# Performance work log

Measured on AMD Instinct MI355X. Metric: run time of the kernel, lower is better.

The kernel has to match this reference:

```python
import jax, jax.numpy as jnp
import numpy as np

D_MODEL = 1024
HIDDEN = 1024
N_EXPERTS = 8
TOP_K = 2
BATCH, SEQ = 2, 2048
N_TOKENS = BATCH * SEQ


def setup_inputs() -> dict:
    key = jax.random.key(0)
    ks = jax.random.split(key, 6)
    x = jax.random.normal(ks[0], (BATCH, SEQ, D_MODEL), dtype=jnp.float32)
    expert_weights = jax.random.uniform(ks[1], (N_TOKENS, TOP_K), dtype=jnp.float32)
    expert_indices = jax.random.randint(ks[2], (N_TOKENS, TOP_K), 0, N_EXPERTS, dtype=jnp.int32)
    s_in = 1.0 / np.sqrt(D_MODEL)
    s_hid = 1.0 / np.sqrt(HIDDEN)
    w1 = jax.random.normal(ks[3], (N_EXPERTS, D_MODEL, HIDDEN), dtype=jnp.float32) * s_in
    w3 = jax.random.normal(ks[4], (N_EXPERTS, D_MODEL, HIDDEN), dtype=jnp.float32) * s_in
    w2 = jax.random.normal(ks[5], (N_EXPERTS, HIDDEN, D_MODEL), dtype=jnp.float32) * s_hid
    return {"x": x, "expert_weights": expert_weights, "expert_indices": expert_indices,
            "w1": w1, "w3": w3, "w2": w2}


def reference(x, expert_weights, expert_indices, w1, w3, w2):
    """Dropless MoE MLP (forward_once path): for each token t,
    out[t] = sum_k expert_weights[t,k] * SwiGLU_{expert_indices[t,k]}(x[t]).
    Also returns batch_size_per_expert (histogram of routed assignments).
    """
    d = x.shape[-1]
    xf = x.reshape(-1, d)                                  # [N, d]
    E = w1.shape[0]
    # combine[t, e] = sum over top-k slots routed to expert e of their weight
    onehot = jax.nn.one_hot(expert_indices, E, dtype=xf.dtype)       # [N, K, E]
    combine = jnp.einsum("nk,nke->ne", expert_weights, onehot)      # [N, E]
    out = jnp.zeros_like(xf)
    for e in range(E):  # fixed small loop over experts
        h = jax.nn.silu(xf @ w1[e]) * (xf @ w3[e])          # [N, H]
        out = out + combine[:, e:e + 1] * (h @ w2[e])       # [N, d]
    batch_size_per_expert = jnp.zeros((E,), dtype=jnp.int32).at[
        expert_indices.reshape(-1)].add(1)
    return out.reshape(x.shape), batch_size_per_expert
```

## Files before the change

kernel.cpp:

```cpp
#include <hip/hip_runtime.h>
#include <cstdint>

#define D 1024
#define N_TOKENS 4096
#define N_SLOTS 8192
#define NEXP 8
#define NKT 16
#define MAXT 80
#define NTRF 8

typedef float f32x4 __attribute__((ext_vector_type(4)));
typedef __bf16 bf16x8 __attribute__((ext_vector_type(8)));
typedef __attribute__((address_space(3))) uint32_t lds_u32;
typedef __attribute__((address_space(1))) const uint32_t glb_u32;

__device__ __forceinline__ void gload_lds16(const void* g, void* l) {
  __builtin_amdgcn_global_load_lds((glb_u32*)g, (lds_u32*)l, 16, 0, 0);
}

__device__ __forceinline__ ushort f2bf(float f) {
  union { float f; uint32_t u; } c; c.f = f;
  uint32_t u = c.u;
  return (ushort)((u + 0x7FFFu + ((u >> 16) & 1u)) >> 16);
}

__device__ __forceinline__ float bf2f(ushort u) {
  union { uint32_t u; float f; } c; c.u = (uint32_t)u << 16;
  return c.f;
}

__device__ __forceinline__ bf16x8 lds_frag(const ushort* base, int row, int s) {
  return *(const bf16x8*)((const char*)base + row * 128 + ((s ^ (row & 7)) * 16));
}

#define TPAD 66

__global__ void prep_k(const float* __restrict__ x, const int* __restrict__ ei,
                       const float* __restrict__ ew,
                       const float* __restrict__ w1, const float* __restrict__ w3,
                       float* __restrict__ hist_out, int* __restrict__ meta,
                       int* __restrict__ tok, int* __restrict__ smap,
                       ushort* __restrict__ Xbf, ushort* __restrict__ w13t) {
  int bid = blockIdx.x, t = threadIdx.x;
  if (bid == 0) {
    __shared__ int cmat[256][8];
    __shared__ int off[NEXP + 1];
#pragma unroll
    for (int e = 0; e < NEXP; e++) cmat[t][e] = 0;
    int base = t * 32;
#pragma unroll 4
    for (int j = 0; j < 32; j++) cmat[t][ei[base + j]]++;
    __syncthreads();
    if (t < NEXP) {
      int run = 0;
      for (int i = 0; i < 256; i++) { int v = cmat[i][t]; cmat[i][t] = run; run += v; }
      meta[8 + t] = run;
    }
    __syncthreads();
    if (t == 0) {
      int s = 0;
      for (int e = 0; e < NEXP; e++) { off[e] = s; s += meta[8 + e]; }
      off[NEXP] = s;
      int nt = 0;
      for (int e = 0; e < NEXP; e++)
        for (int r = off[e]; r < off[e + 1]; r += 128)
          if (nt < MAXT) {
            meta[16 + nt] = e;
            meta[96 + nt] = r;
            int re = off[e + 1]; if (r + 128 < re) re = r + 128;
            meta[176 + nt] = re;
            nt++;
          }
      meta[0] = nt;
      for (int e = 0; e < NEXP; e++) hist_out[e] = (float)meta[8 + e];
    }
    __syncthreads();
#pragma unroll 4
    for (int j = 0; j < 32; j++) {
      int slot = base + j;
      int e = ei[slot];
      int p = off[e] + cmat[t][e]++;
      tok[p] = slot >> 1;
      smap[slot] = p;
    }
  } else if (bid <= 256) {
    int cb = bid - 1;
    const float4* xs = (const float4*)x + (size_t)cb * 4096;
    ushort4* xd = (ushort4*)Xbf + (size_t)cb * 4096;
#pragma unroll
    for (int i = 0; i < 16; i++) {
      float4 v = xs[i * 256 + t];
      ushort4 o;
      o.x = f2bf(v.x); o.y = f2bf(v.y); o.z = f2bf(v.z); o.w = f2bf(v.w);
      xd[i * 256 + t] = o;
    }
  } else {
    int wb = bid - 257;
    int z = wb >> 8, rem = wb & 255;
    int kb = rem >> 4, nb = rem & 15;
    int which = z >> 3, e = z & 7;
    const float* src = (which == 0 ? w1 : w3) + (size_t)e * D * D;
    ushort* dst = w13t + (size_t)e * 2048 * D;
    __shared__ ushort tile[64][TPAD];
    int k0 = kb * 64, n0 = nb * 64;
    int r = t >> 4, c = t & 15;
#pragma unroll
    for (int rep = 0; rep < 4; rep++) {
      int krow = rep * 16 + r;
      float4 v = *(const float4*)(src + (size_t)(k0 + krow) * D + n0 + c * 4);
      tile[krow][c * 4 + 0] = f2bf(v.x);
      tile[krow][c * 4 + 1] = f2bf(v.y);
      tile[krow][c * 4 + 2] = f2bf(v.z);
      tile[krow][c * 4 + 3] = f2bf(v.w);
    }
    __syncthreads();
#pragma unroll
    for (int rep = 0; rep < 4; rep++) {
      int lr = rep * 16 + r;
      int nrow = n0 + lr;
      ushort4 o;
      o.x = tile[c * 4 + 0][lr];
      o.y = tile[c * 4 + 1][lr];
      o.z = tile[c * 4 + 2][lr];
      o.w = tile[c * 4 + 3][lr];
      int crow = ((nrow >> 4) << 5) + ((which == 1) ? 16 : 0) + (nrow & 15);
      *(ushort4*)(dst + (size_t)crow * D + k0 + c * 4) = o;
    }
  }
}

__global__ __launch_bounds__(256, 4) void gemm1_k(
    const ushort* __restrict__ Xbf, const ushort* __restrict__ W13t,
    ushort* __restrict__ H, const int* __restrict__ tok,
    const int* __restrict__ meta,
    const float* __restrict__ w2, ushort* __restrict__ W2t) {
  __shared__ ushort sA[128 * 64];
  __shared__ ushort sB[128 * 64];
  int tm = blockIdx.y;
  int tid = threadIdx.x;

  if (tm < NTRF) {
    int gid = tm * 16 + blockIdx.x;
    int e = gid >> 4, kb = gid & 15;
    const float* src = w2 + (size_t)e * D * D;
    ushort* dst = W2t + (size_t)e * D * D;
    ushort (*tile)[TPAD] = (ushort(*)[TPAD])&sA[0];
    int r = tid >> 4, c = tid & 15;
    int k0 = kb * 64;
    const float* sp = src + (size_t)k0 * D + c * 4;
    float4 va[4], vb[4];
#pragma unroll
    for (int rep = 0; rep < 4; rep++)
      va[rep] = *(const float4*)(sp + (size_t)(rep * 16 + r) * D);
    for (int i = 0; i < 16; i += 2) {
      __syncthreads();
#pragma unroll
      for (int rep = 0; rep < 4; rep++) {
        int krow = rep * 16 + r;
        tile[krow][c * 4 + 0] = f2bf(va[rep].x);
        tile[krow][c * 4 + 1] = f2bf(va[rep].y);
        tile[krow][c * 4 + 2] = f2bf(va[rep].z);
        tile[krow][c * 4 + 3] = f2bf(va[rep].w);
      }
      if (i + 1 < 16)
#pragma unroll
        for (int rep = 0; rep < 4; rep++)
          vb[rep] = *(const float4*)(sp + (size_t)(rep * 16 + r) * D + (i + 1) * 64);
      __syncthreads();
      {
        int n0 = i * 64;
#pragma unroll
        for (int rep = 0; rep < 4; rep++) {
          int lr = rep * 16 + r;
          ushort4 o;
          o.x = tile[c * 4 + 0][lr];
          o.y = tile[c * 4 + 1][lr];
          o.z = tile[c * 4 + 2][lr];
          o.w = tile[c * 4 + 3][lr];
          *(ushort4*)(dst + (size_t)(n0 + lr) * D + k0 + c * 4) = o;
        }
      }
      __syncthreads();
#pragma unroll
      for (int rep = 0; rep < 4; rep++) {
        int krow = rep * 16 + r;
        tile[krow][c * 4 + 0] = f2bf(vb[rep].x);
        tile[krow][c * 4 + 1] = f2bf(vb[rep].y);
        tile[krow][c * 4 + 2] = f2bf(vb[rep].z);
        tile[krow][c * 4 + 3] = f2bf(vb[rep].w);
      }
      if (i + 2 < 16)
#pragma unroll
        for (int rep = 0; rep < 4; rep++)
          va[rep] = *(const float4*)(sp + (size_t)(rep * 16 + r) * D + (i + 2) * 64);
      __syncthreads();
      {
        int n0 = (i + 1) * 64;
#pragma unroll
        for (int rep = 0; rep < 4; rep++) {
          int lr = rep * 16 + r;
          ushort4 o;
          o.x = tile[c * 4 + 0][lr];
          o.y = tile[c * 4 + 1][lr];
          o.z = tile[c * 4 + 2][lr];
          o.w = tile[c * 4 + 3][lr];
          *(ushort4*)(dst + (size_t)(n0 + lr) * D + k0 + c * 4) = o;
        }
      }
    }
    return;
  }
  tm -= NTRF;
  if (tm >= meta[0]) return;

  int e = meta[16 + tm], r0 = meta[96 + tm], rend = meta[176 + tm];
  int n0i = blockIdx.x * 128;
  int lane = tid & 63, wid = tid >> 6;
  int wm = wid >> 1, wn = wid & 1;

  const char* gX = (const char*)Xbf;
  const char* gB = (const char*)(W13t + (size_t)e * 2048 * D);

  int prow = tid >> 3, pslot = tid & 7;
  size_t arow[4];
  int brow[4], phys[4];
#pragma unroll
  for (int i = 0; i < 4; i++) {
    int row = i * 32 + prow;
    int gr = r0 + row; if (gr > N_SLOTS - 1) gr = N_SLOTS - 1;
    arow[i] = (size_t)tok[gr] * 2048;
    brow[i] = n0i + row;
    phys[i] = (pslot ^ (row & 7)) * 16;
  }

  f32x4 acc[4][4] = {};

  for (int kt = 0; kt < NKT; kt++) {
    int kb = kt * 128;
#pragma unroll
    for (int i = 0; i < 4; i++) {
      gload_lds16(gX + arow[i] + kb + phys[i], (char*)sA + (i * 256 + tid) * 16);
      gload_lds16(gB + (size_t)brow[i] * 2048 + kb + phys[i],
                  (char*)sB + (i * 256 + tid) * 16);
    }
    __syncthreads();
#pragma unroll
    for (int kk = 0; kk < 2; kk++) {
      int s = kk * 4 + (lane >> 4);
      bf16x8 a[4], b[4];
#pragma unroll
      for (int mf = 0; mf < 4; mf++)
        a[mf] = lds_frag(sA, wm * 64 + mf * 16 + (lane & 15), s);
#pragma unroll
      for (int nf = 0; nf < 4; nf++)
        b[nf] = lds_frag(sB, wn * 64 + nf * 16 + (lane & 15), s);
#pragma unroll
      for (int mf = 0; mf < 4; mf++)
#pragma unroll
        for (int nf = 0; nf < 4; nf++)
          acc[mf][nf] = __builtin_amdgcn_mfma_f32_16x16x32_bf16(a[mf], b[nf], acc[mf][nf], 0, 0, 0);
    }
    __syncthreads();
  }

  int cb = (n0i >> 1) + wn * 32 + (lane & 15);
#pragma unroll
  for (int mf = 0; mf < 4; mf++)
#pragma unroll
    for (int v = 0; v < 4; v++) {
      int r = r0 + wm * 64 + mf * 16 + (lane >> 4) * 4 + v;
      if (r >= rend) continue;
#pragma unroll
      for (int p = 0; p < 2; p++) {
        float g = acc[mf][2 * p][v], u = acc[mf][2 * p + 1][v];
        float hv = g / (1.f + __expf(-g)) * u;
        H[(size_t)r * D + cb + p * 16] = f2bf(hv);
      }
    }
}

__global__ __launch_bounds__(256, 4) void gemm2_k(
    const ushort* __restrict__ Hm, const ushort* __restrict__ W2t,
    ushort* __restrict__ Y, const int* __restrict__ meta) {
  __shared__ ushort sA[128 * 64];
  __shared__ ushort sB[128 * 64];
  int tm = blockIdx.y;
  if (tm >= meta[0]) return;
  int e = meta[16 + tm], r0 = meta[96 + tm], rend = meta[176 + tm];
  int n0 = blockIdx.x * 128;
  int tid = threadIdx.x, lane = tid & 63, wid = tid >> 6;
  int wm = wid >> 1, wn = wid & 1;

  const char* gH = (const char*)Hm;
  const char* gB = (const char*)(W2t + (size_t)e * D * D);

  int prow = tid >> 3, pslot = tid & 7;
  size_t arow[4];
  int brow[4], phys[4];
#pragma unroll
  for (int i = 0; i < 4; i++) {
    int row = i * 32 + prow;
    int gr = r0 + row; if (gr > N_SLOTS - 1) gr = N_SLOTS - 1;
    arow[i] = (size_t)gr * 2048;
    brow[i] = n0 + row;
    phys[i] = (pslot ^ (row & 7)) * 16;
  }

  f32x4 acc[4][4] = {};

  for (int kt = 0; kt < NKT; kt++) {
    int kb = kt * 128;
#pragma unroll
    for (int i = 0; i < 4; i++) {
      gload_lds16(gH + arow[i] + kb + phys[i], (char*)sA + (i * 256 + tid) * 16);
      gload_lds16(gB + (size_t)brow[i] * 2048 + kb + phys[i],
                  (char*)sB + (i * 256 + tid) * 16);
    }
    __syncthreads();
#pragma unroll
    for (int kk = 0; kk < 2; kk++) {
      int s = kk * 4 + (lane >> 4);
      bf16x8 a[4], b[4];
#pragma unroll
      for (int mf = 0; mf < 4; mf++)
        a[mf] = lds_frag(sA, wm * 64 + mf * 16 + (lane & 15), s);
#pragma unroll
      for (int nf = 0; nf < 4; nf++)
        b[nf] = lds_frag(sB, wn * 64 + nf * 16 + (lane & 15), s);
#pragma unroll
      for (int mf = 0; mf < 4; mf++)
#pragma unroll
        for (int nf = 0; nf < 4; nf++)
          acc[mf][nf] = __builtin_amdgcn_mfma_f32_16x16x32_bf16(a[mf], b[nf], acc[mf][nf], 0, 0, 0);
    }
    __syncthreads();
  }

#pragma unroll
  for (int mf = 0; mf < 4; mf++)
#pragma unroll
    for (int v = 0; v < 4; v++) {
      int r = r0 + wm * 64 + mf * 16 + (lane >> 4) * 4 + v;
      if (r >= rend) continue;
#pragma unroll
      for (int nf = 0; nf < 4; nf++)
        Y[(size_t)r * D + n0 + wn * 64 + nf * 16 + (lane & 15)] = f2bf(acc[mf][nf][v]);
    }
}

__global__ void combine_k(const ushort* __restrict__ Y, const int* __restrict__ smap,
                          const float* __restrict__ ew, float* __restrict__ out) {
  int tkn = blockIdx.x * 4 + (threadIdx.x >> 6);
  int lane = threadIdx.x & 63;
  int p0 = smap[2 * tkn], p1 = smap[2 * tkn + 1];
  float w0 = ew[2 * tkn], w1 = ew[2 * tkn + 1];
  const ushort4* y0 = (const ushort4*)(Y + (size_t)p0 * D);
  const ushort4* y1 = (const ushort4*)(Y + (size_t)p1 * D);
  float4* o = (float4*)(out + (size_t)tkn * D);
#pragma unroll
  for (int j = 0; j < 4; j++) {
    int c = j * 64 + lane;
    ushort4 a = y0[c], b = y1[c];
    float4 v;
    v.x = w0 * bf2f(a.x) + w1 * bf2f(b.x);
    v.y = w0 * bf2f(a.y) + w1 * bf2f(b.y);
    v.z = w0 * bf2f(a.z) + w1 * bf2f(b.z);
    v.w = w0 * bf2f(a.w) + w1 * bf2f(b.w);
    o[c] = v;
  }
}

extern "C" void kernel_launch(void* const* d_in, const int* in_sizes, int n_in,
                              void* d_out, int out_size, void* d_ws, size_t ws_size,
                              hipStream_t stream) {
  const float* x  = (const float*)d_in[0];
  const float* ew = (const float*)d_in[1];
  const int*   ei = (const int*)d_in[2];
  const float* w1 = (const float*)d_in[3];
  const float* w3 = (const float*)d_in[4];
  const float* w2 = (const float*)d_in[5];
  float* out = (float*)d_out;

  char* ws = (char*)d_ws;
  int*    meta = (int*)ws;
  int*    tok  = (int*)(ws + 4096);
  int*    smap = (int*)(ws + 4096 + 32768);
  ushort* Xbf  = (ushort*)(ws + (1ull << 20));
  ushort* W13t = (ushort*)(ws + (9ull << 20));
  ushort* W2t  = (ushort*)(ws + (41ull << 20));
  ushort* Hm   = (ushort*)(ws + (57ull << 20));
  ushort* Ym   = (ushort*)(ws + (1ull << 20));

  prep_k<<<4353, 256, 0, stream>>>(x, ei, ew, w1, w3,
                                   out + (size_t)N_TOKENS * D, meta, tok, smap,
                                   Xbf, W13t);
  gemm1_k<<<dim3(16, NTRF + MAXT), 256, 0, stream>>>(Xbf, W13t, Hm, tok, meta, w2, W2t);
  gemm2_k<<<dim3(8, MAXT), 256, 0, stream>>>(Hm, W2t, Ym, meta);
  combine_k<<<N_TOKENS / 4, 256, 0, stream>>>(Ym, smap, ew, out);
}
```

Measured before the change: 115.5 us.

## Use 256-row tiles with double-buffered split-phase LDS prefetch in MoE GEMMs

Both grouped GEMMs now use 512-thread blocks with 256-row M tiles, and gemm2 also widens its N tile to 256. Global-to-LDS loads are double-buffered in two half-phases with explicit vmcnt waits, raw barriers and setprio, so loads for the next K step overlap MFMA work. The W2 transpose blocks each handle two jobs to match the larger block size. The aim is more data reuse per tile and hidden load latency, at the cost of fewer blocks, fewer waves per CU and more padding waste on partial expert tiles.

```diff
diff --git a/kernel.cpp b/kernel.cpp
--- a/kernel.cpp
+++ b/kernel.cpp
@@ -6,8 +6,8 @@
 #define N_SLOTS 8192
 #define NEXP 8
 #define NKT 16
-#define MAXT 80
-#define NTRF 8
+#define MAXT 40
+#define TRROWS 4
 
 typedef float f32x4 __attribute__((ext_vector_type(4)));
 typedef __bf16 bf16x8 __attribute__((ext_vector_type(8)));
@@ -63,11 +63,11 @@
       off[NEXP] = s;
       int nt = 0;
       for (int e = 0; e < NEXP; e++)
-        for (int r = off[e]; r < off[e + 1]; r += 128)
+        for (int r = off[e]; r < off[e + 1]; r += 256)
           if (nt < MAXT) {
             meta[16 + nt] = e;
             meta[96 + nt] = r;
-            int re = off[e + 1]; if (r + 128 < re) re = r + 128;
+            int re = off[e + 1]; if (r + 256 < re) re = r + 256;
             meta[176 + nt] = re;
             nt++;
           }
@@ -129,23 +129,24 @@
   }
 }
 
-__global__ __launch_bounds__(256, 4) void gemm1_k(
+__global__ __launch_bounds__(512, 2) void gemm1_k(
     const ushort* __restrict__ Xbf, const ushort* __restrict__ W13t,
     ushort* __restrict__ H, const int* __restrict__ tok,
     const int* __restrict__ meta,
     const float* __restrict__ w2, ushort* __restrict__ W2t) {
-  __shared__ ushort sA[128 * 64];
-  __shared__ ushort sB[128 * 64];
+  __shared__ ushort L[2][24576];
   int tm = blockIdx.y;
   int tid = threadIdx.x;
 
-  if (tm < NTRF) {
-    int gid = tm * 16 + blockIdx.x;
-    int e = gid >> 4, kb = gid & 15;
+  if (tm >= MAXT) {
+    int gid = (tm - MAXT) * 16 + blockIdx.x;
+    int half = tid >> 8, t8 = tid & 255;
+    int job = gid * 2 + half;
+    int e = job >> 4, kb = job & 15;
     const float* src = w2 + (size_t)e * D * D;
     ushort* dst = W2t + (size_t)e * D * D;
-    ushort (*tile)[TPAD] = (ushort(*)[TPAD])&sA[0];
-    int r = tid >> 4, c = tid & 15;
+    ushort (*tile)[TPAD] = (ushort(*)[TPAD])(&L[0][0] + half * 4224);
+    int r = t8 >> 4, c = t8 & 15;
     int k0 = kb * 64;
     const float* sp = src + (size_t)k0 * D + c * 4;
     float4 va[4], vb[4];
@@ -210,142 +211,181 @@
     }
     return;
   }
-  tm -= NTRF;
   if (tm >= meta[0]) return;
 
   int e = meta[16 + tm], r0 = meta[96 + tm], rend = meta[176 + tm];
   int n0i = blockIdx.x * 128;
   int lane = tid & 63, wid = tid >> 6;
-  int wm = wid >> 1, wn = wid & 1;
+  int wm = wid >> 2, wn = wid & 3;
 
   const char* gX = (const char*)Xbf;
   const char* gB = (const char*)(W13t + (size_t)e * 2048 * D);
 
   int prow = tid >> 3, pslot = tid & 7;
+  int phys = (pslot ^ (prow & 7)) * 16;
   size_t arow[4];
-  int brow[4], phys[4];
-#pragma unroll
-  for (int i = 0; i < 4; i++) {
-    int row = i * 32 + prow;
-    int gr = r0 + row; if (gr > N_SLOTS - 1) gr = N_SLOTS - 1;
-    arow[i] = (size_t)tok[gr] * 2048;
-    brow[i] = n0i + row;
-    phys[i] = (pslot ^ (row & 7)) * 16;
-  }
-
-  f32x4 acc[4][4] = {};
-
+  int brow[2];
+#pragma unroll
+  for (int g = 0; g < 4; g++) {
+    int gr = r0 + g * 64 + prow; if (gr > N_SLOTS - 1) gr = N_SLOTS - 1;
+    arow[g] = (size_t)tok[gr] * 2048;
+  }
+#pragma unroll
+  for (int g = 0; g < 2; g++) brow[g] = n0i + g * 64 + prow;
+
+#define G1A(c, g, kB) gload_lds16(gX + arow[g] + (kB) + phys, \
+    (char*)&L[c][0] + ((g) * 512 + tid) * 16)
+#define G1B(c, g, kB) gload_lds16(gB + (size_t)brow[g] * 2048 + (kB) + phys, \
+    (char*)&L[c][0] + 32768 + ((g) * 512 + tid) * 16)
+#define G1H0(c, kB) { G1A(c, 0, kB); G1A(c, 1, kB); G1B(c, 0, kB); }
+#define G1H1(c, kB) { G1A(c, 2, kB); G1A(c, 3, kB); G1B(c, 1, kB); }
+
+  f32x4 acc[8][2] = {};
+
+  G1H0(0, 0); G1H1(0, 0);
+  G1H0(1, 128);
+  asm volatile("s_waitcnt vmcnt(3)" ::: "memory");
+  __builtin_amdgcn_s_barrier();
+  __builtin_amdgcn_sched_barrier(0);
+
+  int cur = 0;
   for (int kt = 0; kt < NKT; kt++) {
-    int kb = kt * 128;
-#pragma unroll
-    for (int i = 0; i < 4; i++) {
-      gload_lds16(gX + arow[i] + kb + phys[i], (char*)sA + (i * 256 + tid) * 16);
-      gload_lds16(gB + (size_t)brow[i] * 2048 + kb + phys[i],
-                  (char*)sB + (i * 256 + tid) * 16);
-    }
-    __syncthreads();
+    if (kt + 1 < NKT) G1H1(cur ^ 1, (kt + 1) * 128);
+    const ushort* Ab = &L[cur][0];
+    const ushort* Bb = &L[cur][16384];
+    __builtin_amdgcn_s_setprio(1);
 #pragma unroll
     for (int kk = 0; kk < 2; kk++) {
       int s = kk * 4 + (lane >> 4);
-      bf16x8 a[4], b[4];
-#pragma unroll
-      for (int mf = 0; mf < 4; mf++)
-        a[mf] = lds_frag(sA, wm * 64 + mf * 16 + (lane & 15), s);
-#pragma unroll
-      for (int nf = 0; nf < 4; nf++)
-        b[nf] = lds_frag(sB, wn * 64 + nf * 16 + (lane & 15), s);
-#pragma unroll
-      for (int mf = 0; mf < 4; mf++)
-#pragma unroll
-        for (int nf = 0; nf < 4; nf++)
-          acc[mf][nf] = __builtin_amdgcn_mfma_f32_16x16x32_bf16(a[mf], b[nf], acc[mf][nf], 0, 0, 0);
-    }
-    __syncthreads();
-  }
-
-  int cb = (n0i >> 1) + wn * 32 + (lane & 15);
-#pragma unroll
-  for (int mf = 0; mf < 4; mf++)
+      bf16x8 b0 = lds_frag(Bb, wn * 32 + (lane & 15), s);
+      bf16x8 b1 = lds_frag(Bb, wn * 32 + 16 + (lane & 15), s);
+#pragma unroll
+      for (int mf = 0; mf < 8; mf++) {
+        bf16x8 a = lds_frag(Ab, wm * 128 + mf * 16 + (lane & 15), s);
+        acc[mf][0] = __builtin_amdgcn_mfma_f32_16x16x32_bf16(a, b0, acc[mf][0], 0, 0, 0);
+        acc[mf][1] = __builtin_amdgcn_mfma_f32_16x16x32_bf16(a, b1, acc[mf][1], 0, 0, 0);
+      }
+    }
+    __builtin_amdgcn_s_setprio(0);
+    __builtin_amdgcn_s_barrier();
+    __builtin_amdgcn_sched_barrier(0);
+    if (kt + 2 < NKT) {
+      G1H0(cur, (kt + 2) * 128);
+      asm volatile("s_waitcnt vmcnt(3)" ::: "memory");
+    } else {
+      asm volatile("s_waitcnt vmcnt(0)" ::: "memory");
+    }
+    __builtin_amdgcn_s_barrier();
+    __builtin_amdgcn_sched_barrier(0);
+    cur ^= 1;
+  }
+
+  int cb = (n0i >> 1) + wn * 16 + (lane & 15);
+#pragma unroll
+  for (int mf = 0; mf < 8; mf++)
 #pragma unroll
     for (int v = 0; v < 4; v++) {
-      int r = r0 + wm * 64 + mf * 16 + (lane >> 4) * 4 + v;
+      int r = r0 + wm * 128 + mf * 16 + (lane >> 4) * 4 + v;
       if (r >= rend) continue;
-#pragma unroll
-      for (int p = 0; p < 2; p++) {
-        float g = acc[mf][2 * p][v], u = acc[mf][2 * p + 1][v];
-        float hv = g / (1.f + __expf(-g)) * u;
-        H[(size_t)r * D + cb + p * 16] = f2bf(hv);
-      }
-    }
-}
-
-__global__ __launch_bounds__(256, 4) void gemm2_k(
+      float g = acc[mf][0][v], u = acc[mf][1][v];
+      float hv = g / (1.f + __expf(-g)) * u;
+      H[(size_t)r * D + cb] = f2bf(hv);
+    }
+#undef G1A
+#undef G1B
+#undef G1H0
+#undef G1H1
+}
+
+__global__ __launch_bounds__(512, 2) void gemm2_k(
     const ushort* __restrict__ Hm, const ushort* __restrict__ W2t,
     ushort* __restrict__ Y, const int* __restrict__ meta) {
-  __shared__ ushort sA[128 * 64];
-  __shared__ ushort sB[128 * 64];
+  __shared__ ushort L[2][32768];
   int tm = blockIdx.y;
   if (tm >= meta[0]) return;
   int e = meta[16 + tm], r0 = meta[96 + tm], rend = meta[176 + tm];
-  int n0 = blockIdx.x * 128;
+  int n0 = blockIdx.x * 256;
   int tid = threadIdx.x, lane = tid & 63, wid = tid >> 6;
-  int wm = wid >> 1, wn = wid & 1;
+  int wm = wid >> 2, wn = wid & 3;
 
   const char* gH = (const char*)Hm;
   const char* gB = (const char*)(W2t + (size_t)e * D * D);
 
   int prow = tid >> 3, pslot = tid & 7;
+  int phys = (pslot ^ (prow & 7)) * 16;
   size_t arow[4];
-  int brow[4], phys[4];
-#pragma unroll
-  for (int i = 0; i < 4; i++) {
-    int row = i * 32 + prow;
-    int gr = r0 + row; if (gr > N_SLOTS - 1) gr = N_SLOTS - 1;
-    arow[i] = (size_t)gr * 2048;
-    brow[i] = n0 + row;
-    phys[i] = (pslot ^ (row & 7)) * 16;
-  }
-
-  f32x4 acc[4][4] = {};
-
+  int brow[4];
+#pragma unroll
+  for (int g = 0; g < 4; g++) {
+    int gr = r0 + g * 64 + prow; if (gr > N_SLOTS - 1) gr = N_SLOTS - 1;
+    arow[g] = (size_t)gr * 2048;
+    brow[g] = n0 + g * 64 + prow;
+  }
+
+#define G2A(c, g, kB) gload_lds16(gH + arow[g] + (kB) + phys, \
+    (char*)&L[c][0] + ((g) * 512 + tid) * 16)
+#define G2B(c, g, kB) gload_lds16(gB + (size_t)brow[g] * 2048 + (kB) + phys, \
+    (char*)&L[c][0] + 32768 + ((g) * 512 + tid) * 16)
+#define G2H0(c, kB) { G2A(c, 0, kB); G2A(c, 1, kB); G2B(c, 0, kB); G2B(c, 1, kB); }
+#define G2H1(c, kB) { G2A(c, 2, kB); G2A(c, 3, kB); G2B(c, 2, kB); G2B(c, 3, kB); }
+
+  f32x4 acc[8][4] = {};
+
+  G2H0(0, 0); G2H1(0, 0);
+  G2H0(1, 128);
+  asm volatile("s_waitcnt vmcnt(4)" ::: "memory");
+  __builtin_amdgcn_s_barrier();
+  __builtin_amdgcn_sched_barrier(0);
+
+  int cur = 0;
   for (int kt = 0; kt < NKT; kt++) {
-    int kb = kt * 128;
-#pragma unroll
-    for (int i = 0; i < 4; i++) {
-      gload_lds16(gH + arow[i] + kb + phys[i], (char*)sA + (i * 256 + tid) * 16);
-      gload_lds16(gB + (size_t)brow[i] * 2048 + kb + phys[i],
-                  (char*)sB + (i * 256 + tid) * 16);
-    }
-    __syncthreads();
+    if (kt + 1 < NKT) G2H1(cur ^ 1, (kt + 1) * 128);
+    const ushort* Ab = &L[cur][0];
+    const ushort* Bb = &L[cur][16384];
+    __builtin_amdgcn_s_setprio(1);
 #pragma unroll
     for (int kk = 0; kk < 2; kk++) {
       int s = kk * 4 + (lane >> 4);
-      bf16x8 a[4], b[4];
-#pragma unroll
-      for (int mf = 0; mf < 4; mf++)
-        a[mf] = lds_frag(sA, wm * 64 + mf * 16 + (lane & 15), s);
+      bf16x8 b[4];
 #pragma unroll
       for (int nf = 0; nf < 4; nf++)
-        b[nf] = lds_frag(sB, wn * 64 + nf * 16 + (lane & 15), s);
-#pragma unroll
-      for (int mf = 0; mf < 4; mf++)
+        b[nf] = lds_frag(Bb, wn * 64 + nf * 16 + (lane & 15), s);
+#pragma unroll
+      for (int mf = 0; mf < 8; mf++) {
+        bf16x8 a = lds_frag(Ab, wm * 128 + mf * 16 + (lane & 15), s);
 #pragma unroll
         for (int nf = 0; nf < 4; nf++)
-          acc[mf][nf] = __builtin_amdgcn_mfma_f32_16x16x32_bf16(a[mf], b[nf], acc[mf][nf], 0, 0, 0);
-    }
-    __syncthreads();
-  }
-
-#pragma unroll
-  for (int mf = 0; mf < 4; mf++)
+          acc[mf][nf] = __builtin_amdgcn_mfma_f32_16x16x32_bf16(a, b[nf], acc[mf][nf], 0, 0, 0);
+      }
+    }
+    __builtin_amdgcn_s_setprio(0);
+    __builtin_amdgcn_s_barrier();
+    __builtin_amdgcn_sched_barrier(0);
+    if (kt + 2 < NKT) {
+      G2H0(cur, (kt + 2) * 128);
+      asm volatile("s_waitcnt vmcnt(4)" ::: "memory");
+    } else {
+      asm volatile("s_waitcnt vmcnt(0)" ::: "memory");
+    }
+    __builtin_amdgcn_s_barrier();
+    __builtin_amdgcn_sched_barrier(0);
+    cur ^= 1;
+  }
+
+#pragma unroll
+  for (int mf = 0; mf < 8; mf++)
 #pragma unroll
     for (int v = 0; v < 4; v++) {
-      int r = r0 + wm * 64 + mf * 16 + (lane >> 4) * 4 + v;
+      int r = r0 + wm * 128 + mf * 16 + (lane >> 4) * 4 + v;
       if (r >= rend) continue;
 #pragma unroll
       for (int nf = 0; nf < 4; nf++)
         Y[(size_t)r * D + n0 + wn * 64 + nf * 16 + (lane & 15)] = f2bf(acc[mf][nf][v]);
     }
+#undef G2A
+#undef G2B
+#undef G2H0
+#undef G2H1
 }
 
 __global__ void combine_k(const ushort* __restrict__ Y, const int* __restrict__ smap,
@@ -394,7 +434,7 @@
   prep_k<<<4353, 256, 0, stream>>>(x, ei, ew, w1, w3,
                                    out + (size_t)N_TOKENS * D, meta, tok, smap,
                                    Xbf, W13t);
-  gemm1_k<<<dim3(16, NTRF + MAXT), 256, 0, stream>>>(Xbf, W13t, Hm, tok, meta, w2, W2t);
-  gemm2_k<<<dim3(8, MAXT), 256, 0, stream>>>(Hm, W2t, Ym, meta);
+  gemm1_k<<<dim3(16, MAXT + TRROWS), 512, 0, stream>>>(Xbf, W13t, Hm, tok, meta, w2, W2t);
+  gemm2_k<<<dim3(4, MAXT), 512, 0, stream>>>(Hm, W2t, Ym, meta);
   combine_k<<<N_TOKENS / 4, 256, 0, stream>>>(Ym, smap, ew, out);
 }
```

Measured after the change: 121.1 us. +4.8%, slower.
